# Optimization experiments

Hardware: AMD Instinct MI355X
Metric: run time of the kernel (lower is better)

Reference implementation:

```python
import jax, jax.numpy as jnp
import numpy as np

N, E, L, F, M = 512, 2048, 16, 16, 8
HOPS = 2      # egonet radius (k_hop_subgraph num_hops)
H = 128       # WL hash buckets
N_ITER = 3    # WeisfeilerLehman(n_iter=3)
TAU = 0.1     # soft-relabeling temperature


def setup_inputs():
    key = jax.random.key(0)
    k0, k1, k2, k3, k4, k5 = jax.random.split(key, 6)
    labels = jax.random.randint(k0, (N,), 0, L)
    x = jax.nn.one_hot(labels, L, dtype=jnp.float32)
    edge_index = jax.random.randint(k1, (2, E), 0, N)
    # filter adjacencies, built exactly as in GKernel.__init__:
    # symmetric 0/1 with zero diagonal
    A = jax.random.uniform(k2, (F, M, M))
    A = ((A + jnp.swapaxes(A, -1, -2)) > 1.0).astype(jnp.float32)
    A = A * (1.0 - jnp.eye(M, dtype=jnp.float32))
    Xlab = jax.random.randint(k3, (F, M), 0, L)
    X = jax.nn.one_hot(Xlab, L, dtype=jnp.float32)
    # injective label -> bucket embedding (random distinct buckets)
    E0 = jax.nn.one_hot(jax.random.permutation(k4, H)[:L], H, dtype=jnp.float32)
    # random projection used to hash (own-label, neighbor-multiset) signatures
    Rproj = jax.random.normal(k5, (2 * H, H), dtype=jnp.float32)
    return {"x": x, "edge_index": edge_index, "P": A, "X": X, "E0": E0, "Rproj": Rproj}


def _wl_features(c0, nbr_sum, mask, Rproj):
    # soft Weisfeiler-Lehman subtree features: at each iteration the new
    # node label is a hash of (own label, neighbor-label multiset); the
    # graph feature is the concatenated per-iteration label histograms.
    c = c0 * mask[:, None]                       # [n, H]
    feats = [c.sum(0)]
    for _ in range(N_ITER):
        sig = jnp.concatenate([c, nbr_sum(c)], axis=-1)        # [n, 2H]
        c = jax.nn.softmax((sig @ Rproj) / TAU, axis=-1) * mask[:, None]
        feats.append(c.sum(0))
    return jnp.concatenate(feats)                # [(N_ITER+1)*H]


def _max_comp_mask(A):
    # largest connected component via min-label propagation (max_comp)
    comp = jnp.arange(M, dtype=jnp.float32)
    Ab = A > 0
    for _ in range(M):
        nbr_min = jnp.min(jnp.where(Ab, comp[None, :], 1e9), axis=1)
        comp = jnp.minimum(comp, nbr_min)
    ci = comp.astype(jnp.int32)
    counts = jax.ops.segment_sum(jnp.ones(M, jnp.float32), ci, num_segments=M)
    best = jnp.argmax(counts)
    return (ci == best).astype(jnp.float32)


def reference(x, edge_index, P, X, E0, Rproj):
    # symmetrize edges (egonets / WL kernels are undirected)
    src = jnp.concatenate([edge_index[0], edge_index[1]])
    dst = jnp.concatenate([edge_index[1], edge_index[0]])
    # --- k-hop egonet node masks (compute_egonets) : reach[i, j] = 1 iff
    # node j is within HOPS hops of root i ---
    reach = jnp.eye(N, dtype=jnp.float32)
    for _ in range(HOPS):
        agg = jax.ops.segment_sum(reach[:, src].T, dst, num_segments=N).T
        reach = jnp.clip(reach + agg, 0.0, 1.0)
    c0 = x @ E0                                  # initial bucket labels [N, H]

    def ego_feat(mask):
        emask = (mask[src] * mask[dst])[:, None]
        def nbr(c):
            return jax.ops.segment_sum(c[src] * emask, dst, num_segments=N)
        return _wl_features(c0, nbr, mask, Rproj)

    ego_feats = jax.vmap(ego_feat)(reach)        # [N, (N_ITER+1)*H]

    def filt_feat(Af, Xf):
        mask = _max_comp_mask(Af)
        Am = Af * mask[:, None] * mask[None, :]
        return _wl_features(Xf @ E0, lambda c: Am @ c, mask, Rproj)

    filt_feats = jax.vmap(filt_feat)(P, X)       # [F, (N_ITER+1)*H]

    # normalized WL kernel: k(g1,g2)/sqrt(k(g1,g1) k(g2,g2)); sim.T -> [N, F]
    sim = filt_feats @ ego_feats.T               # [F, N]
    nf = jnp.linalg.norm(filt_feats, axis=-1)
    ng = jnp.linalg.norm(ego_feats, axis=-1)
    sim = sim / (nf[:, None] * ng[None, :] + 1e-12)
    return sim.T
```

## Files before the change

### kernel.cpp

```cpp
#include <hip/hip_runtime.h>
#include <hip/hip_bf16.h>

#define NN 512
#define EE 2048
#define LL 16
#define FF 16
#define MM 8
#define HH 128
#define CAP_ROWS 40960
#define MAXD 32
#define TAU_SCALE 14.426950408889634f

typedef float v2f __attribute__((ext_vector_type(2)));

constexpr size_t OFF_ADJ   = 0;
constexpr size_t SZ_ADJ    = (size_t)NN * 8 * 8;
constexpr size_t OFF_DEG   = OFF_ADJ + SZ_ADJ;
constexpr size_t SZ_DEG    = (size_t)NN * 4;
constexpr size_t OFF_CNT   = OFF_DEG + SZ_DEG;
constexpr size_t SZ_CNT    = (size_t)NN * 4;
constexpr size_t OFF_ROFF  = OFF_CNT + SZ_CNT;
constexpr size_t SZ_ROFF   = (size_t)(NN + 1) * 4 + 12;
constexpr size_t OFF_BUCKN = OFF_ROFF + SZ_ROFF;
constexpr size_t SZ_BUCKN  = (size_t)NN * 4;
constexpr size_t OFF_BUCKF = OFF_BUCKN + SZ_BUCKN;
constexpr size_t SZ_BUCKF  = (size_t)FF * MM * 4;
constexpr size_t OFF_NLST  = ((OFF_BUCKF + SZ_BUCKF + 63) / 64) * 64;
constexpr size_t SZ_NLST   = (size_t)NN * MAXD * 2;
constexpr size_t OFF_CEGO  = OFF_NLST + SZ_NLST;
constexpr size_t SZ_CEGO   = (size_t)CAP_ROWS * 2;
constexpr size_t OFF_NCNT  = OFF_CEGO + SZ_CEGO;
constexpr size_t SZ_NCNT   = (size_t)CAP_ROWS * 2;
constexpr size_t OFF_RBK   = OFF_NCNT + SZ_NCNT;
constexpr size_t SZ_RBK    = (size_t)CAP_ROWS * 2;
constexpr size_t OFF_NBR   = OFF_RBK + SZ_RBK;
constexpr size_t SZ_NBR    = (size_t)CAP_ROWS * MAXD * 2;
constexpr size_t OFF_NBK   = OFF_NBR + SZ_NBR;
constexpr size_t SZ_NBK    = (size_t)CAP_ROWS * MAXD * 2;
constexpr size_t OFF_EGOF  = ((OFF_NBK + SZ_NBK + 63) / 64) * 64;
constexpr size_t SZ_EGOF   = (size_t)NN * 512 * 4;
constexpr size_t OFF_FILTF = OFF_EGOF + SZ_EGOF;
constexpr size_t SZ_FILTF  = (size_t)FF * 512 * 4;
constexpr size_t OFF_FNORM = OFF_FILTF + SZ_FILTF;
constexpr size_t SZ_FNORM  = 64;
constexpr size_t OFF_CA    = ((OFF_FNORM + SZ_FNORM + 255) / 256) * 256;
constexpr size_t SZ_CBUF   = (size_t)CAP_ROWS * HH * 4;
constexpr size_t OFF_CB    = OFF_CA + SZ_CBUF;

__global__ __launch_bounds__(256) void k_build(const int* __restrict__ ei,
                                               const float* __restrict__ x,
                                               const float* __restrict__ X,
                                               const float* __restrict__ E0,
                                               int* __restrict__ degN,
                                               unsigned short* __restrict__ nbrLstN,
                                               unsigned long long* __restrict__ adj,
                                               int* __restrict__ buckN,
                                               int* __restrict__ buckF) {
    int idx = blockIdx.x * blockDim.x + threadIdx.x;
    if (idx < EE) {
        int a = ei[idx], b = ei[EE + idx];
        int p = atomicAdd(&degN[a], 1);
        if (p < MAXD) nbrLstN[(size_t)a * MAXD + p] = (unsigned short)b;
        int q = atomicAdd(&degN[b], 1);
        if (q < MAXD) nbrLstN[(size_t)b * MAXD + q] = (unsigned short)a;
        atomicOr(&adj[(size_t)a * 8 + (b >> 6)], 1ull << (b & 63));
        atomicOr(&adj[(size_t)b * 8 + (a >> 6)], 1ull << (a & 63));
    } else if (idx < EE + NN) {
        int i = idx - EE;
        int lab = 0;
        for (int l = 0; l < LL; ++l) if (x[i * LL + l] > 0.5f) lab = l;
        int b = 0;
        for (int h = 0; h < HH; ++h) if (E0[lab * HH + h] > 0.5f) b = h;
        buckN[i] = b;
    } else if (idx < EE + NN + FF * MM) {
        int fm = idx - EE - NN;
        int lab = 0;
        for (int l = 0; l < LL; ++l) if (X[fm * LL + l] > 0.5f) lab = l;
        int b = 0;
        for (int h = 0; h < HH; ++h) if (E0[lab * HH + h] > 0.5f) b = h;
        buckF[fm] = b;
    }
}

__global__ __launch_bounds__(64) void k_reach(const unsigned long long* __restrict__ adj,
                                              unsigned long long* __restrict__ bitsR,
                                              int* __restrict__ count) {
    __shared__ unsigned long long r1[8];
    __shared__ unsigned long long r2[8];
    int i = blockIdx.x, t = threadIdx.x;
    if (t < 8) {
        unsigned long long v = adj[(size_t)i * 8 + t];
        if (t == (i >> 6)) v |= 1ull << (i & 63);
        r1[t] = v;
        r2[t] = v;
    }
    __syncthreads();
    unsigned long long p[8] = {0, 0, 0, 0, 0, 0, 0, 0};
    for (int rep = 0; rep < 8; ++rep) {
        if ((r1[rep] >> t) & 1ull) {
            int j = t + rep * 64;
#pragma unroll
            for (int w = 0; w < 8; ++w) p[w] |= adj[(size_t)j * 8 + w];
        }
    }
#pragma unroll
    for (int w = 0; w < 8; ++w)
        if (p[w]) atomicOr(&r2[w], p[w]);
    __syncthreads();
    if (t < 8) bitsR[(size_t)i * 8 + t] = r2[t];
    if (t == 0) {
        int acc = 0;
        for (int w = 0; w < 8; ++w) acc += __popcll(r2[w]);
        count[i] = acc;
    }
}

__global__ __launch_bounds__(512) void k_scan(const int* __restrict__ in,
                                              int* __restrict__ out) {
    __shared__ int s[NN];
    int t = threadIdx.x;
    s[t] = in[t];
    __syncthreads();
    for (int d = 1; d < NN; d <<= 1) {
        int v = (t >= d) ? s[t - d] : 0;
        __syncthreads();
        s[t] += v;
        __syncthreads();
    }
    out[t + 1] = s[t];
    if (t == 0) out[0] = 0;
}

__global__ __launch_bounds__(64) void k_pack(const unsigned long long* __restrict__ bitsR,
                                             const int* __restrict__ count,
                                             const int* __restrict__ rowOff,
                                             const int* __restrict__ degN,
                                             const unsigned short* __restrict__ nbrLstN,
                                             const int* __restrict__ buckN,
                                             unsigned short* __restrict__ nbrRow,
                                             unsigned short* __restrict__ nbrBuck,
                                             unsigned short* __restrict__ nbrCnt,
                                             unsigned short* __restrict__ rowBuck,
                                             unsigned short* __restrict__ cegoG,
                                             float* __restrict__ egoF) {
    __shared__ unsigned long long bits[8];
    __shared__ int wpre[8];
    __shared__ unsigned short cmap_s[NN];
    __shared__ unsigned short nodes_s[NN];
    __shared__ float f0[HH];
    int i = blockIdx.x, t = threadIdx.x;
    if (t < 8) bits[t] = bitsR[(size_t)i * 8 + t];
    if (t < 64) { f0[t] = 0.0f; f0[t + 64] = 0.0f; }
    __syncthreads();
    if (t == 0) {
        int acc = 0;
        for (int w = 0; w < 8; ++w) { wpre[w] = acc; acc += __popcll(bits[w]); }
    }
    __syncthreads();
    int base = rowOff[i];
    int n = count[i];
    if (base >= CAP_ROWS) n = 0;
    else if (base + n > CAP_ROWS) n = CAP_ROWS - base;
    for (int rep = 0; rep < 8; ++rep) {
        int j = t + rep * 64;
        unsigned long long word = bits[rep];
        unsigned short v = 0xFFFFu;
        if ((word >> t) & 1ull) {
            int idx = wpre[rep] + __popcll(word & ((1ull << t) - 1ull));
            if (idx < n) { v = (unsigned short)idx; nodes_s[idx] = (unsigned short)j; }
        }
        cmap_s[j] = v;
    }
    for (int q = 256 + t; q < 512; q += 64) egoF[(size_t)i * 512 + q] = 0.0f;
    __syncthreads();
    for (int m = t; m < n; m += 64) {
        int j = nodes_s[m];
        int b = buckN[j];
        atomicAdd(&f0[b], 1.0f);
        size_t row = (size_t)(base + m);
        rowBuck[row] = (unsigned short)b;
        int dn = degN[j]; if (dn > MAXD) dn = MAXD;
        int cnt = 0;
        for (int e = 0; e < dn; ++e) {
            unsigned short nbNode = nbrLstN[(size_t)j * MAXD + e];
            unsigned short nr = cmap_s[nbNode];
            if (nr != 0xFFFFu && cnt < MAXD) {
                nbrRow[row * MAXD + cnt] = (unsigned short)(base + nr);
                nbrBuck[row * MAXD + cnt] = (unsigned short)buckN[nbNode];
                cnt++;
            }
        }
        nbrCnt[row] = (unsigned short)cnt;
        cegoG[row] = (unsigned short)i;
    }
    __syncthreads();
    if (t < 64) {
        egoF[(size_t)i * 512 + t] = f0[t];
        egoF[(size_t)i * 512 + t + 64] = f0[t + 64];
    }
}

__global__ __launch_bounds__(256) void k_iter1(const int* __restrict__ count,
                                               const int* __restrict__ rowOff,
                                               const unsigned short* __restrict__ rowBuck,
                                               const unsigned short* __restrict__ nbrBuck,
                                               const unsigned short* __restrict__ nbrCnt,
                                               const float* __restrict__ Rg,
                                               float* __restrict__ cOut,
                                               float* __restrict__ egoF) {
    __shared__ float fs[HH];
    int i = blockIdx.x, tid = threadIdx.x;
    int base = rowOff[i];
    int n = count[i];
    if (base >= CAP_ROWS) n = 0;
    else if (base + n > CAP_ROWS) n = CAP_ROWS - base;
    if (tid < HH) fs[tid] = 0.0f;
    __syncthreads();
    const float* Rb = Rg + (size_t)HH * HH;
    int col = (tid & 7) * 16;
    float facc[16];
#pragma unroll
    for (int q = 0; q < 16; ++q) facc[q] = 0.0f;
    for (int m = tid >> 3; m < n; m += 32) {
        int gr = base + m;
        float z[16];
        const float* rt = Rg + (size_t)rowBuck[gr] * HH + col;
#pragma unroll
        for (int q = 0; q < 4; ++q) *(float4*)&z[q * 4] = *(const float4*)&rt[q * 4];
        int cnt = nbrCnt[gr];
        const unsigned short* nk = &nbrBuck[(size_t)gr * MAXD];
        for (int e = 0; e < cnt; ++e) {
            const float* rb = Rb + (size_t)nk[e] * HH + col;
#pragma unroll
            for (int q = 0; q < 4; ++q) {
                float4 rv = *(const float4*)&rb[q * 4];
                z[q * 4 + 0] += rv.x; z[q * 4 + 1] += rv.y;
                z[q * 4 + 2] += rv.z; z[q * 4 + 3] += rv.w;
            }
        }
        float mx = z[0];
#pragma unroll
        for (int q = 1; q < 16; ++q) mx = fmaxf(mx, z[q]);
        for (int off = 4; off > 0; off >>= 1) mx = fmaxf(mx, __shfl_xor(mx, off));
        float s = 0.0f;
#pragma unroll
        for (int q = 0; q < 16; ++q) { z[q] = exp2f((z[q] - mx) * TAU_SCALE); s += z[q]; }
        for (int off = 4; off > 0; off >>= 1) s += __shfl_xor(s, off);
        float inv = 1.0f / s;
        float* crow = cOut + (size_t)gr * HH + col;
#pragma unroll
        for (int q = 0; q < 16; ++q) { z[q] *= inv; facc[q] += z[q]; }
#pragma unroll
        for (int q = 0; q < 4; ++q) *(float4*)&crow[q * 4] = *(const float4*)&z[q * 4];
    }
#pragma unroll
    for (int q = 0; q < 16; ++q) atomicAdd(&fs[col + q], facc[q]);
    __syncthreads();
    if (tid < HH) egoF[(size_t)i * 512 + HH + tid] = fs[tid];
}

__global__ __launch_bounds__(64) void k_iter(const float* __restrict__ cur,
                                             float* __restrict__ nxt,
                                             const float* __restrict__ Rg,
                                             const int* __restrict__ rowOff,
                                             const unsigned short* __restrict__ nbrRow,
                                             const unsigned short* __restrict__ nbrCnt,
                                             const unsigned short* __restrict__ cegoG,
                                             float* __restrict__ egoF,
                                             int it) {
    __shared__ __align__(16) float cs[8][HH];
    __shared__ __align__(16) float us[8][HH];
    int Rtot = rowOff[NN];
    if (Rtot > CAP_ROWS) Rtot = CAP_ROWS;
    int r0 = blockIdx.x * 8;
    if (r0 >= Rtot) return;
    int tid = threadIdx.x;
    for (int q = 0; q < 4; ++q) {
        int idx = q * 64 + tid;
        int row = idx >> 5, col = (idx & 31) << 2;
        int gr = r0 + row; if (gr >= Rtot) gr = Rtot - 1;
        *(float4*)&cs[row][col] = *(const float4*)&cur[(size_t)gr * HH + col];
    }
    {
        int row = tid >> 3;
        int gr = r0 + row;
        int col = (tid & 7) * 16;
        float4 a0 = make_float4(0.f, 0.f, 0.f, 0.f);
        float4 a1 = a0, a2 = a0, a3 = a0;
        if (gr < Rtot) {
            int cnt = nbrCnt[gr];
            const unsigned short* nb = &nbrRow[(size_t)gr * MAXD];
            for (int e = 0; e < cnt; ++e) {
                const float4* cr = (const float4*)&cur[(size_t)nb[e] * HH + col];
                float4 b0 = cr[0], b1 = cr[1], b2 = cr[2], b3 = cr[3];
                a0.x += b0.x; a0.y += b0.y; a0.z += b0.z; a0.w += b0.w;
                a1.x += b1.x; a1.y += b1.y; a1.z += b1.z; a1.w += b1.w;
                a2.x += b2.x; a2.y += b2.y; a2.z += b2.z; a2.w += b2.w;
                a3.x += b3.x; a3.y += b3.y; a3.z += b3.z; a3.w += b3.w;
            }
        }
        float4* up = (float4*)&us[row][col];
        up[0] = a0; up[1] = a1; up[2] = a2; up[3] = a3;
    }
    __syncthreads();
    v2f acc[8];
#pragma unroll
    for (int j = 0; j < 8; ++j) acc[j] = (v2f)(0.0f);
    int h2 = 2 * tid;
    const float* Rb = Rg + (size_t)HH * HH;
#pragma unroll 4
    for (int k = 0; k < HH; k += 4) {
        v2f rv0 = *(const v2f*)&Rg[(size_t)(k + 0) * HH + h2];
        v2f rv1 = *(const v2f*)&Rg[(size_t)(k + 1) * HH + h2];
        v2f rv2 = *(const v2f*)&Rg[(size_t)(k + 2) * HH + h2];
        v2f rv3 = *(const v2f*)&Rg[(size_t)(k + 3) * HH + h2];
#pragma unroll
        for (int j = 0; j < 8; ++j) {
            float4 cv = *(const float4*)&cs[j][k];
            acc[j] += cv.x * rv0;
            acc[j] += cv.y * rv1;
            acc[j] += cv.z * rv2;
            acc[j] += cv.w * rv3;
        }
    }
#pragma unroll 4
    for (int k = 0; k < HH; k += 4) {
        v2f rv0 = *(const v2f*)&Rb[(size_t)(k + 0) * HH + h2];
        v2f rv1 = *(const v2f*)&Rb[(size_t)(k + 1) * HH + h2];
        v2f rv2 = *(const v2f*)&Rb[(size_t)(k + 2) * HH + h2];
        v2f rv3 = *(const v2f*)&Rb[(size_t)(k + 3) * HH + h2];
#pragma unroll
        for (int j = 0; j < 8; ++j) {
            float4 uv = *(const float4*)&us[j][k];
            acc[j] += uv.x * rv0;
            acc[j] += uv.y * rv1;
            acc[j] += uv.z * rv2;
            acc[j] += uv.w * rv3;
        }
    }
    int cege = -1;
    float fa0 = 0.f, fa1 = 0.f;
#pragma unroll
    for (int j = 0; j < 8; ++j) {
        int gr = r0 + j;
        if (gr < Rtot) {
            float a0 = acc[j].x, a1 = acc[j].y;
            float m = fmaxf(a0, a1);
            for (int off = 32; off > 0; off >>= 1) m = fmaxf(m, __shfl_xor(m, off));
            float e0 = exp2f((a0 - m) * TAU_SCALE);
            float e1 = exp2f((a1 - m) * TAU_SCALE);
            float s = e0 + e1;
            for (int off = 32; off > 0; off >>= 1) s += __shfl_xor(s, off);
            float inv = 1.0f / s;
            float c0 = e0 * inv, c1 = e1 * inv;
            *(float2*)&nxt[(size_t)gr * HH + h2] = make_float2(c0, c1);
            int ego = cegoG[gr];
            if (ego != cege) {
                if (cege >= 0) {
                    atomicAdd(&egoF[(size_t)cege * 512 + it * HH + h2], fa0);
                    atomicAdd(&egoF[(size_t)cege * 512 + it * HH + h2 + 1], fa1);
                }
                cege = ego; fa0 = 0.f; fa1 = 0.f;
            }
            fa0 += c0; fa1 += c1;
        }
    }
    if (cege >= 0) {
        atomicAdd(&egoF[(size_t)cege * 512 + it * HH + h2], fa0);
        atomicAdd(&egoF[(size_t)cege * 512 + it * HH + h2 + 1], fa1);
    }
}

__global__ __launch_bounds__(256) void k_filt(const float* __restrict__ P,
                                              const int* __restrict__ buckF,
                                              const float* __restrict__ Rg,
                                              float* __restrict__ filtF,
                                              float* __restrict__ fnorm) {
    __shared__ float As[MM][MM];
    __shared__ float Am[MM][MM];
    __shared__ float msk[MM];
    __shared__ float cbuf[2][MM][HH];
    __shared__ float ubuf[MM][HH];
    __shared__ float feats[4 * HH];
    __shared__ float red4[4];
    int f = blockIdx.x, tid = threadIdx.x, wave = tid >> 6, lane = tid & 63;
    if (tid < 64) As[tid >> 3][tid & 7] = P[f * 64 + tid];
    for (int idx = tid; idx < 4 * HH; idx += 256) feats[idx] = 0.f;
    __syncthreads();
    if (tid == 0) {
        float comp[MM];
        for (int m = 0; m < MM; ++m) comp[m] = (float)m;
        for (int it = 0; it < MM; ++it) {
            float nm[MM];
            for (int j = 0; j < MM; ++j) {
                float mn = 1e9f;
                for (int k = 0; k < MM; ++k)
                    if (As[j][k] > 0.f) mn = fminf(mn, comp[k]);
                nm[j] = mn;
            }
            for (int j = 0; j < MM; ++j) comp[j] = fminf(comp[j], nm[j]);
        }
        int cnt[MM], ci[MM];
        for (int m = 0; m < MM; ++m) cnt[m] = 0;
        for (int m = 0; m < MM; ++m) { ci[m] = (int)comp[m]; cnt[ci[m]]++; }
        int best = 0;
        for (int m = 1; m < MM; ++m) if (cnt[m] > cnt[best]) best = m;
        for (int m = 0; m < MM; ++m) msk[m] = (ci[m] == best) ? 1.0f : 0.0f;
    }
    __syncthreads();
    if (tid < 64) Am[tid >> 3][tid & 7] = As[tid >> 3][tid & 7] * msk[tid >> 3] * msk[tid & 7];
    for (int idx = tid; idx < MM * HH; idx += 256) {
        int m = idx >> 7, h = idx & 127;
        cbuf[0][m][h] = (msk[m] > 0.f && h == buckF[f * MM + m]) ? 1.0f : 0.0f;
    }
    __syncthreads();
    if (tid < HH) {
        float s = 0.f;
        for (int m = 0; m < MM; ++m) s += cbuf[0][m][tid];
        feats[tid] = s;
    }
    __syncthreads();
    int cur = 0;
    int h2 = 2 * lane;
    for (int it = 1; it <= 3; ++it) {
#pragma unroll
        for (int jj = 0; jj < 2; ++jj) {
            int d = wave * 2 + jj;
            float u0 = 0.f, u1 = 0.f;
            for (int s = 0; s < MM; ++s) {
                float w = Am[d][s];
                u0 += w * cbuf[cur][s][h2];
                u1 += w * cbuf[cur][s][h2 + 1];
            }
            ubuf[d][h2] = u0;
            ubuf[d][h2 + 1] = u1;
        }
        float a0[2] = {0.f, 0.f}, a1[2] = {0.f, 0.f};
        for (int k = 0; k < HH; ++k) {
            float2 rt = *(const float2*)&Rg[(size_t)k * HH + h2];
            float2 rb = *(const float2*)&Rg[(size_t)(HH + k) * HH + h2];
#pragma unroll
            for (int jj = 0; jj < 2; ++jj) {
                int d = wave * 2 + jj;
                float cd = cbuf[cur][d][k];
                float ud = ubuf[d][k];
                a0[jj] += cd * rt.x + ud * rb.x;
                a1[jj] += cd * rt.y + ud * rb.y;
            }
        }
#pragma unroll
        for (int jj = 0; jj < 2; ++jj) {
            int d = wave * 2 + jj;
            float z0 = a0[jj], z1 = a1[jj];
            float m = fmaxf(z0, z1);
            for (int off = 32; off > 0; off >>= 1) m = fmaxf(m, __shfl_xor(m, off));
            float e0 = exp2f((z0 - m) * TAU_SCALE);
            float e1 = exp2f((z1 - m) * TAU_SCALE);
            float s = e0 + e1;
            for (int off = 32; off > 0; off >>= 1) s += __shfl_xor(s, off);
            float inv = msk[d] / s;
            float c0 = e0 * inv, c1 = e1 * inv;
            cbuf[1 - cur][d][h2] = c0;
            cbuf[1 - cur][d][h2 + 1] = c1;
            atomicAdd(&feats[it * HH + h2], c0);
            atomicAdd(&feats[it * HH + h2 + 1], c1);
        }
        __syncthreads();
        cur = 1 - cur;
    }
    float np = 0.f;
    for (int idx = tid; idx < 4 * HH; idx += 256) {
        float v = feats[idx];
        filtF[(size_t)f * 512 + idx] = v;
        np += v * v;
    }
    for (int off = 32; off > 0; off >>= 1) np += __shfl_xor(np, off);
    if (lane == 0) red4[wave] = np;
    __syncthreads();
    if (tid == 0) fnorm[f] = sqrtf(red4[0] + red4[1] + red4[2] + red4[3]);
}

__global__ __launch_bounds__(64) void k_sim(const float* __restrict__ egoF,
                                            const float* __restrict__ filtF,
                                            const float* __restrict__ fnorm,
                                            float* __restrict__ out) {
    int i = blockIdx.x, lane = threadIdx.x;
    float e[8];
    float ss = 0.f;
#pragma unroll
    for (int r = 0; r < 8; ++r) {
        e[r] = egoF[(size_t)i * 512 + r * 64 + lane];
        ss += e[r] * e[r];
    }
    for (int off = 32; off > 0; off >>= 1) ss += __shfl_xor(ss, off);
    float ng = sqrtf(ss);
    for (int f = 0; f < FF; ++f) {
        float d = 0.f;
#pragma unroll
        for (int r = 0; r < 8; ++r) d += e[r] * filtF[(size_t)f * 512 + r * 64 + lane];
        for (int off = 32; off > 0; off >>= 1) d += __shfl_xor(d, off);
        if (lane == 0) out[i * FF + f] = d / (fnorm[f] * ng + 1e-12f);
    }
}

extern "C" void kernel_launch(void* const* d_in, const int* in_sizes, int n_in,
                              void* d_out, int out_size, void* d_ws, size_t ws_size,
                              hipStream_t stream) {
    (void)in_sizes; (void)n_in; (void)out_size; (void)ws_size;
    const float* x  = (const float*)d_in[0];
    const int*   ei = (const int*)d_in[1];
    const float* P  = (const float*)d_in[2];
    const float* X  = (const float*)d_in[3];
    const float* E0 = (const float*)d_in[4];
    const float* Rg = (const float*)d_in[5];
    float* out = (float*)d_out;
    char* ws = (char*)d_ws;

    unsigned long long* adj   = (unsigned long long*)(ws + OFF_ADJ);
    int* degN   = (int*)(ws + OFF_DEG);
    int* count  = (int*)(ws + OFF_CNT);
    int* rowOff = (int*)(ws + OFF_ROFF);
    int* buckN  = (int*)(ws + OFF_BUCKN);
    int* buckF  = (int*)(ws + OFF_BUCKF);
    unsigned short* nbrLstN = (unsigned short*)(ws + OFF_NLST);
    unsigned short* cego    = (unsigned short*)(ws + OFF_CEGO);
    unsigned short* nbrCnt  = (unsigned short*)(ws + OFF_NCNT);
    unsigned short* rowBuck = (unsigned short*)(ws + OFF_RBK);
    unsigned short* nbrRow  = (unsigned short*)(ws + OFF_NBR);
    unsigned short* nbrBuck = (unsigned short*)(ws + OFF_NBK);
    float* egoF  = (float*)(ws + OFF_EGOF);
    float* filtF = (float*)(ws + OFF_FILTF);
    float* fnorm = (float*)(ws + OFF_FNORM);
    float* cA    = (float*)(ws + OFF_CA);
    float* cB    = (float*)(ws + OFF_CB);
    unsigned long long* bitsR = (unsigned long long*)(ws + OFF_CA);

    hipMemsetAsync(ws, 0, OFF_CNT, stream);
    k_build<<<(EE + NN + FF * MM + 255) / 256, 256, 0, stream>>>(ei, x, X, E0, degN, nbrLstN,
                                                                 adj, buckN, buckF);
    k_reach<<<NN, 64, 0, stream>>>(adj, bitsR, count);
    k_scan<<<1, 512, 0, stream>>>(count, rowOff);
    k_pack<<<NN, 64, 0, stream>>>(bitsR, count, rowOff, degN, nbrLstN, buckN,
                                  nbrRow, nbrBuck, nbrCnt, rowBuck, cego, egoF);
    k_iter1<<<NN, 256, 0, stream>>>(count, rowOff, rowBuck, nbrBuck, nbrCnt, Rg, cB, egoF);
    k_iter<<<CAP_ROWS / 8, 64, 0, stream>>>(cB, cA, Rg, rowOff, nbrRow, nbrCnt, cego, egoF, 2);
    k_iter<<<CAP_ROWS / 8, 64, 0, stream>>>(cA, cB, Rg, rowOff, nbrRow, nbrCnt, cego, egoF, 3);
    k_filt<<<FF, 256, 0, stream>>>(P, buckF, Rg, filtF, fnorm);
    k_sim<<<NN, 64, 0, stream>>>(egoF, filtF, fnorm, out);
}
```

Measured before the change: 303.5 us.

## Use split-bf16 MFMA for WL iteration projection with 16-row tiles

Replaces the scalar FP32 sig@Rproj product in k_iter with MFMA 16x16x32 bf16 instructions. To keep near-FP32 accuracy it uses a hi/lo bf16 split of both operands (three MFMAs per tile). A new k_prep kernel transposes Rproj and splits it into hi/lo bf16 arrays, stored in the no-longer-used nbrBuck workspace region. Each block now covers 16 rows, and neighbor sums are gathered directly into registers instead of shared memory. The softmax is reduced across the MFMA output layout. The risks are the extra conversion work, lower precision of the split approximation, and reuse of the nbrBuck workspace.

```diff
diff --git a/kernel.cpp b/kernel.cpp
--- a/kernel.cpp
+++ b/kernel.cpp
@@ -11,7 +11,8 @@
 #define MAXD 32
 #define TAU_SCALE 14.426950408889634f
 
-typedef float v2f __attribute__((ext_vector_type(2)));
+typedef __attribute__((ext_vector_type(8))) short bf16x8;
+typedef __attribute__((ext_vector_type(4))) float f32x4;
 
 constexpr size_t OFF_ADJ   = 0;
 constexpr size_t SZ_ADJ    = (size_t)NN * 8 * 8;
@@ -47,6 +48,12 @@
 constexpr size_t SZ_CBUF   = (size_t)CAP_ROWS * HH * 4;
 constexpr size_t OFF_CB    = OFF_CA + SZ_CBUF;
 
+__device__ __forceinline__ unsigned f2bfbits(float x) {
+    unsigned u = __float_as_uint(x);
+    return (u + 0x7fffu + ((u >> 16) & 1u)) >> 16;
+}
+__device__ __forceinline__ float bf2f(unsigned hb) { return __uint_as_float(hb << 16); }
+
 __global__ __launch_bounds__(256) void k_build(const int* __restrict__ ei,
                                                const float* __restrict__ x,
                                                const float* __restrict__ X,
@@ -259,115 +266,165 @@
     if (tid < HH) egoF[(size_t)i * 512 + HH + tid] = fs[tid];
 }
 
+__global__ __launch_bounds__(256) void k_prep(const float* __restrict__ Rg,
+                                              short* __restrict__ RtH,
+                                              short* __restrict__ RtL) {
+    int idx = blockIdx.x * blockDim.x + threadIdx.x;
+    int col = idx >> 5;
+    int kc = (idx & 31) * 8;
+    bf16x8 hv, lv;
+#pragma unroll
+    for (int j = 0; j < 8; ++j) {
+        float xv = Rg[(size_t)(kc + j) * HH + col];
+        unsigned hb = f2bfbits(xv);
+        hv[j] = (short)hb;
+        lv[j] = (short)f2bfbits(xv - bf2f(hb));
+    }
+    *(bf16x8*)&RtH[(size_t)col * 256 + kc] = hv;
+    *(bf16x8*)&RtL[(size_t)col * 256 + kc] = lv;
+}
+
 __global__ __launch_bounds__(64) void k_iter(const float* __restrict__ cur,
                                              float* __restrict__ nxt,
-                                             const float* __restrict__ Rg,
+                                             const short* __restrict__ RtH,
+                                             const short* __restrict__ RtL,
                                              const int* __restrict__ rowOff,
                                              const unsigned short* __restrict__ nbrRow,
                                              const unsigned short* __restrict__ nbrCnt,
                                              const unsigned short* __restrict__ cegoG,
                                              float* __restrict__ egoF,
                                              int it) {
-    __shared__ __align__(16) float cs[8][HH];
-    __shared__ __align__(16) float us[8][HH];
     int Rtot = rowOff[NN];
     if (Rtot > CAP_ROWS) Rtot = CAP_ROWS;
-    int r0 = blockIdx.x * 8;
+    int r0 = blockIdx.x * 16;
     if (r0 >= Rtot) return;
     int tid = threadIdx.x;
-    for (int q = 0; q < 4; ++q) {
-        int idx = q * 64 + tid;
-        int row = idx >> 5, col = (idx & 31) << 2;
-        int gr = r0 + row; if (gr >= Rtot) gr = Rtot - 1;
-        *(float4*)&cs[row][col] = *(const float4*)&cur[(size_t)gr * HH + col];
-    }
+    int c16 = tid & 15, g = tid >> 4;
+    int kb = g * 8;
+    int grA = r0 + c16;
+    if (grA >= Rtot) grA = Rtot - 1;
+
+    float ua[4][8];
+#pragma unroll
+    for (int s = 0; s < 4; ++s)
+#pragma unroll
+        for (int j = 0; j < 8; ++j) ua[s][j] = 0.0f;
     {
-        int row = tid >> 3;
-        int gr = r0 + row;
-        int col = (tid & 7) * 16;
-        float4 a0 = make_float4(0.f, 0.f, 0.f, 0.f);
-        float4 a1 = a0, a2 = a0, a3 = a0;
+        int cnt = nbrCnt[grA];
+        const unsigned short* nb = &nbrRow[(size_t)grA * MAXD];
+        for (int e = 0; e < cnt; ++e) {
+            const float* cr = &cur[(size_t)nb[e] * HH + kb];
+#pragma unroll
+            for (int s = 0; s < 4; ++s) {
+                float4 v0 = *(const float4*)&cr[s * 32];
+                float4 v1 = *(const float4*)&cr[s * 32 + 4];
+                ua[s][0] += v0.x; ua[s][1] += v0.y; ua[s][2] += v0.z; ua[s][3] += v0.w;
+                ua[s][4] += v1.x; ua[s][5] += v1.y; ua[s][6] += v1.z; ua[s][7] += v1.w;
+            }
+        }
+    }
+
+    f32x4 acc[8];
+#pragma unroll
+    for (int n = 0; n < 8; ++n) acc[n] = (f32x4)(0.0f);
+    const short* bbH = RtH + (size_t)c16 * 256 + kb;
+    const short* bbL = RtL + (size_t)c16 * 256 + kb;
+
+#pragma unroll
+    for (int s = 0; s < 4; ++s) {
+        bf16x8 ahi, alo;
+#pragma unroll
+        for (int j = 0; j < 8; ++j) {
+            float xv = ua[s][j];
+            unsigned hb = f2bfbits(xv);
+            ahi[j] = (short)hb;
+            alo[j] = (short)f2bfbits(xv - bf2f(hb));
+        }
+        const int t = s + 4;
+#pragma unroll
+        for (int n = 0; n < 8; ++n) {
+            bf16x8 bh = *(const bf16x8*)&bbH[n * 4096 + t * 32];
+            bf16x8 bl = *(const bf16x8*)&bbL[n * 4096 + t * 32];
+            acc[n] = __builtin_amdgcn_mfma_f32_16x16x32_bf16(ahi, bh, acc[n], 0, 0, 0);
+            acc[n] = __builtin_amdgcn_mfma_f32_16x16x32_bf16(ahi, bl, acc[n], 0, 0, 0);
+            acc[n] = __builtin_amdgcn_mfma_f32_16x16x32_bf16(alo, bh, acc[n], 0, 0, 0);
+        }
+    }
+    {
+        const float* cr = &cur[(size_t)grA * HH + kb];
+#pragma unroll
+        for (int t = 0; t < 4; ++t) {
+            float4 v0 = *(const float4*)&cr[t * 32];
+            float4 v1 = *(const float4*)&cr[t * 32 + 4];
+            float cv[8] = {v0.x, v0.y, v0.z, v0.w, v1.x, v1.y, v1.z, v1.w};
+            bf16x8 ahi, alo;
+#pragma unroll
+            for (int j = 0; j < 8; ++j) {
+                unsigned hb = f2bfbits(cv[j]);
+                ahi[j] = (short)hb;
+                alo[j] = (short)f2bfbits(cv[j] - bf2f(hb));
+            }
+#pragma unroll
+            for (int n = 0; n < 8; ++n) {
+                bf16x8 bh = *(const bf16x8*)&bbH[n * 4096 + t * 32];
+                bf16x8 bl = *(const bf16x8*)&bbL[n * 4096 + t * 32];
+                acc[n] = __builtin_amdgcn_mfma_f32_16x16x32_bf16(ahi, bh, acc[n], 0, 0, 0);
+                acc[n] = __builtin_amdgcn_mfma_f32_16x16x32_bf16(ahi, bl, acc[n], 0, 0, 0);
+                acc[n] = __builtin_amdgcn_mfma_f32_16x16x32_bf16(alo, bh, acc[n], 0, 0, 0);
+            }
+        }
+    }
+
+    float inv[4];
+#pragma unroll
+    for (int i = 0; i < 4; ++i) {
+        float m = acc[0][i];
+#pragma unroll
+        for (int n = 1; n < 8; ++n) m = fmaxf(m, acc[n][i]);
+        for (int off = 8; off > 0; off >>= 1) m = fmaxf(m, __shfl_xor(m, off));
+        float s = 0.0f;
+#pragma unroll
+        for (int n = 0; n < 8; ++n) {
+            float e = exp2f((acc[n][i] - m) * TAU_SCALE);
+            acc[n][i] = e; s += e;
+        }
+        for (int off = 8; off > 0; off >>= 1) s += __shfl_xor(s, off);
+        inv[i] = 1.0f / s;
+    }
+
+    float fa[8];
+#pragma unroll
+    for (int n = 0; n < 8; ++n) fa[n] = 0.0f;
+    int cege = -1;
+#pragma unroll
+    for (int i = 0; i < 4; ++i) {
+        int gr = r0 + g * 4 + i;
         if (gr < Rtot) {
-            int cnt = nbrCnt[gr];
-            const unsigned short* nb = &nbrRow[(size_t)gr * MAXD];
-            for (int e = 0; e < cnt; ++e) {
-                const float4* cr = (const float4*)&cur[(size_t)nb[e] * HH + col];
-                float4 b0 = cr[0], b1 = cr[1], b2 = cr[2], b3 = cr[3];
-                a0.x += b0.x; a0.y += b0.y; a0.z += b0.z; a0.w += b0.w;
-                a1.x += b1.x; a1.y += b1.y; a1.z += b1.z; a1.w += b1.w;
-                a2.x += b2.x; a2.y += b2.y; a2.z += b2.z; a2.w += b2.w;
-                a3.x += b3.x; a3.y += b3.y; a3.z += b3.z; a3.w += b3.w;
-            }
-        }
-        float4* up = (float4*)&us[row][col];
-        up[0] = a0; up[1] = a1; up[2] = a2; up[3] = a3;
-    }
-    __syncthreads();
-    v2f acc[8];
-#pragma unroll
-    for (int j = 0; j < 8; ++j) acc[j] = (v2f)(0.0f);
-    int h2 = 2 * tid;
-    const float* Rb = Rg + (size_t)HH * HH;
-#pragma unroll 4
-    for (int k = 0; k < HH; k += 4) {
-        v2f rv0 = *(const v2f*)&Rg[(size_t)(k + 0) * HH + h2];
-        v2f rv1 = *(const v2f*)&Rg[(size_t)(k + 1) * HH + h2];
-        v2f rv2 = *(const v2f*)&Rg[(size_t)(k + 2) * HH + h2];
-        v2f rv3 = *(const v2f*)&Rg[(size_t)(k + 3) * HH + h2];
-#pragma unroll
-        for (int j = 0; j < 8; ++j) {
-            float4 cv = *(const float4*)&cs[j][k];
-            acc[j] += cv.x * rv0;
-            acc[j] += cv.y * rv1;
-            acc[j] += cv.z * rv2;
-            acc[j] += cv.w * rv3;
-        }
-    }
-#pragma unroll 4
-    for (int k = 0; k < HH; k += 4) {
-        v2f rv0 = *(const v2f*)&Rb[(size_t)(k + 0) * HH + h2];
-        v2f rv1 = *(const v2f*)&Rb[(size_t)(k + 1) * HH + h2];
-        v2f rv2 = *(const v2f*)&Rb[(size_t)(k + 2) * HH + h2];
-        v2f rv3 = *(const v2f*)&Rb[(size_t)(k + 3) * HH + h2];
-#pragma unroll
-        for (int j = 0; j < 8; ++j) {
-            float4 uv = *(const float4*)&us[j][k];
-            acc[j] += uv.x * rv0;
-            acc[j] += uv.y * rv1;
-            acc[j] += uv.z * rv2;
-            acc[j] += uv.w * rv3;
-        }
-    }
-    int cege = -1;
-    float fa0 = 0.f, fa1 = 0.f;
-#pragma unroll
-    for (int j = 0; j < 8; ++j) {
-        int gr = r0 + j;
-        if (gr < Rtot) {
-            float a0 = acc[j].x, a1 = acc[j].y;
-            float m = fmaxf(a0, a1);
-            for (int off = 32; off > 0; off >>= 1) m = fmaxf(m, __shfl_xor(m, off));
-            float e0 = exp2f((a0 - m) * TAU_SCALE);
-            float e1 = exp2f((a1 - m) * TAU_SCALE);
-            float s = e0 + e1;
-            for (int off = 32; off > 0; off >>= 1) s += __shfl_xor(s, off);
-            float inv = 1.0f / s;
-            float c0 = e0 * inv, c1 = e1 * inv;
-            *(float2*)&nxt[(size_t)gr * HH + h2] = make_float2(c0, c1);
+#pragma unroll
+            for (int n = 0; n < 8; ++n) {
+                float c = acc[n][i] * inv[i];
+                nxt[(size_t)gr * HH + n * 16 + c16] = c;
+                acc[n][i] = c;
+            }
             int ego = cegoG[gr];
             if (ego != cege) {
                 if (cege >= 0) {
-                    atomicAdd(&egoF[(size_t)cege * 512 + it * HH + h2], fa0);
-                    atomicAdd(&egoF[(size_t)cege * 512 + it * HH + h2 + 1], fa1);
+#pragma unroll
+                    for (int n = 0; n < 8; ++n) {
+                        atomicAdd(&egoF[(size_t)cege * 512 + it * HH + n * 16 + c16], fa[n]);
+                        fa[n] = 0.0f;
+                    }
                 }
-                cege = ego; fa0 = 0.f; fa1 = 0.f;
-            }
-            fa0 += c0; fa1 += c1;
+                cege = ego;
+            }
+#pragma unroll
+            for (int n = 0; n < 8; ++n) fa[n] += acc[n][i];
         }
     }
     if (cege >= 0) {
-        atomicAdd(&egoF[(size_t)cege * 512 + it * HH + h2], fa0);
-        atomicAdd(&egoF[(size_t)cege * 512 + it * HH + h2 + 1], fa1);
+#pragma unroll
+        for (int n = 0; n < 8; ++n)
+            atomicAdd(&egoF[(size_t)cege * 512 + it * HH + n * 16 + c16], fa[n]);
     }
 }
 
@@ -534,6 +591,8 @@
     float* cA    = (float*)(ws + OFF_CA);
     float* cB    = (float*)(ws + OFF_CB);
     unsigned long long* bitsR = (unsigned long long*)(ws + OFF_CA);
+    short* RtH = (short*)(ws + OFF_NBK);
+    short* RtL = RtH + (size_t)HH * 256;
 
     hipMemsetAsync(ws, 0, OFF_CNT, stream);
     k_build<<<(EE + NN + FF * MM + 255) / 256, 256, 0, stream>>>(ei, x, X, E0, degN, nbrLstN,
@@ -543,8 +602,9 @@
     k_pack<<<NN, 64, 0, stream>>>(bitsR, count, rowOff, degN, nbrLstN, buckN,
                                   nbrRow, nbrBuck, nbrCnt, rowBuck, cego, egoF);
     k_iter1<<<NN, 256, 0, stream>>>(count, rowOff, rowBuck, nbrBuck, nbrCnt, Rg, cB, egoF);
-    k_iter<<<CAP_ROWS / 8, 64, 0, stream>>>(cB, cA, Rg, rowOff, nbrRow, nbrCnt, cego, egoF, 2);
-    k_iter<<<CAP_ROWS / 8, 64, 0, stream>>>(cA, cB, Rg, rowOff, nbrRow, nbrCnt, cego, egoF, 3);
+    k_prep<<<16, 256, 0, stream>>>(Rg, RtH, RtL);
+    k_iter<<<CAP_ROWS / 16, 64, 0, stream>>>(cB, cA, RtH, RtL, rowOff, nbrRow, nbrCnt, cego, egoF, 2);
+    k_iter<<<CAP_ROWS / 16, 64, 0, stream>>>(cA, cB, RtH, RtL, rowOff, nbrRow, nbrCnt, cego, egoF, 3);
     k_filt<<<FF, 256, 0, stream>>>(P, buckF, Rg, filtF, fnorm);
     k_sim<<<NN, 64, 0, stream>>>(egoF, filtF, fnorm, out);
 }
```

Measured after the change: 305.7 us. About the same (+0.7%).
